# Kernel optimization log

Hardware: AMD Instinct MI355X
Metric: run time of the kernel (lower is better)

## Reference

```python
import jax, jax.numpy as jnp
import numpy as np

WINDOW_SIZE = 11
SIGMA = 1.5
LEVELS = 5
WEIGHTS = np.array([0.0448, 0.2856, 0.3001, 0.2363, 0.1333], dtype=np.float32)
C1 = 0.01 ** 2  # (0.01 * L)^2, L = 1
C2 = 0.03 ** 2


def _gauss_window(channel):
    x = np.arange(WINDOW_SIZE, dtype=np.float32) - WINDOW_SIZE // 2
    g = np.exp(-x ** 2 / (2.0 * SIGMA ** 2)).astype(np.float32)
    g = g / g.sum()
    w2 = np.outer(g, g)  # [ws, ws]
    w = np.broadcast_to(w2, (channel, 1, WINDOW_SIZE, WINDOW_SIZE)).copy()
    return jnp.asarray(w)


def _dwconv(x, w, channel):
    # depthwise conv, padding=0 (VALID), groups=channel
    return jax.lax.conv_general_dilated(
        x, w, window_strides=(1, 1), padding='VALID',
        dimension_numbers=('NCHW', 'OIHW', 'NCHW'),
        feature_group_count=channel)


def _ssim(img1, img2, window, channel):
    mu1 = _dwconv(img1, window, channel)
    mu2 = _dwconv(img2, window, channel)
    mu1_sq = mu1 * mu1
    mu2_sq = mu2 * mu2
    mu1_mu2 = mu1 * mu2
    sigma1_sq = _dwconv(img1 * img1, window, channel) - mu1_sq
    sigma2_sq = _dwconv(img2 * img2, window, channel) - mu2_sq
    sigma12 = _dwconv(img1 * img2, window, channel) - mu1_mu2
    v1 = 2.0 * sigma12 + C2
    v2 = sigma1_sq + sigma2_sq + C2
    cs = jnp.mean(v1 / v2)
    ssim_map = (2.0 * mu1_mu2 + C1) * v1 / ((mu1_sq + mu2_sq + C1) * v2)
    return jnp.mean(ssim_map), cs


def _avg_pool2(x):
    # avg_pool2d(kernel=2, stride=2), VALID
    s = jax.lax.reduce_window(x, 0.0, jax.lax.add, (1, 1, 2, 2), (1, 1, 2, 2), 'VALID')
    return s * 0.25


def setup_inputs() -> dict:
    key = jax.random.key(0)
    k1, k2 = jax.random.split(key)
    img1 = jax.random.uniform(k1, (16, 3, 512, 512), dtype=jnp.float32)
    img2 = jax.random.uniform(k2, (16, 3, 512, 512), dtype=jnp.float32)
    return {"img1": img1, "img2": img2}


def reference(img1, img2):
    channel = img1.shape[1]
    window = _gauss_window(channel)
    weights = jnp.asarray(WEIGHTS)
    mssim, mcs = [], []
    a, b = img1, img2
    for _ in range(LEVELS):  # fixed pyramid depth, shapes differ per level
        s, c = _ssim(a, b, window, channel)
        mssim.append(s)
        mcs.append(c)
        a = _avg_pool2(a)
        b = _avg_pool2(b)
    mssim = (jnp.stack(mssim) + 1.0) * 0.5  # normalize=True
    mcs = (jnp.stack(mcs) + 1.0) * 0.5
    return jnp.prod(mcs[:-1] ** weights[:-1]) * mssim[-1] ** weights[-1]
```

## Files before the change

### kernel.cpp

```cpp
#include <hip/hip_runtime.h>
#include <math.h>

#define WS 11
#define PAD 10
#define NC 48
#define C1V 1.0e-4f
#define C2V 9.0e-4f
#define PLROWS 42
#define RST 65

typedef float v2f __attribute__((ext_vector_type(2)));

struct Params { float g[WS]; };
struct ROff { int off[5]; int cnt[5]; float inv[5]; };

__device__ __forceinline__ void row_conv_unit(
    const float* __restrict__ rowa, const float* __restrict__ rowb,
    const int xq[4], int cg,
    v2f* __restrict__ rowSD, v2f* __restrict__ rowE2, const Params& P)
{
    v2f msd[4] = {{0,0},{0,0},{0,0},{0,0}};
    v2f me2[4] = {{0,0},{0,0},{0,0},{0,0}};
#pragma unroll
    for (int q = 0; q < 4; ++q) {
        const float4 va = *(const float4*)(rowa + xq[q]);
        const float4 vb = *(const float4*)(rowb + xq[q]);
        const float fa[4] = {va.x, va.y, va.z, va.w};
        const float fb[4] = {vb.x, vb.y, vb.z, vb.w};
#pragma unroll
        for (int e = 0; e < 4; ++e) {
            const int i = q * 4 + e;
            v2f sd; sd.x = fa[e] + fb[e]; sd.y = fa[e] - fb[e];
            const v2f sq = sd * sd;
#pragma unroll
            for (int j = 0; j < 4; ++j) {
                const int k = i - j;
                if (k >= 0 && k < WS) {
                    const float g = P.g[k];
                    msd[j] += g * sd;
                    me2[j] += g * sq;
                }
            }
        }
    }
#pragma unroll
    for (int j = 0; j < 4; ++j) {
        rowSD[cg*4 + j] = msd[j];
        rowE2[cg*4 + j] = me2[j];
    }
}

template<int CH, int POOL>
__global__ __launch_bounds__(512) void ssim_strip_kernel(
    const float* __restrict__ img1, const float* __restrict__ img2,
    float* __restrict__ pool1, float* __restrict__ pool2,
    int H, int OH, int tilesX, Params P,
    float2* __restrict__ partial, int partial_off)
{
    __shared__ v2f rpSD[PLROWS][RST];
    __shared__ v2f rpE2[PLROWS][RST];
    __shared__ float reds[8], redc[8];
    const int tid   = threadIdx.x;
    const int tileX = blockIdx.x % tilesX;
    const int ty    = blockIdx.x / tilesX;
    const int img   = blockIdx.y;
    const size_t ib = (size_t)img * H * H;
    const float* __restrict__ p1 = img1 + ib;
    const float* __restrict__ p2 = img2 + ib;
    const int ox0 = tileX * 64;
    const int oy0 = ty * (CH * 32);

    const int r_unit = tid >> 4;
    const int cg     = tid & 15;
    int xq[4];
#pragma unroll
    for (int q = 0; q < 4; ++q) xq[q] = min(ox0 + cg*4 + q*4, H - 4);

    const int cc  = tid & 63;
    const int r0c = (tid >> 6) * 4;

    if (tid < 160) {
        const int y = min(oy0 + r_unit, H - 1);
        row_conv_unit(p1 + (size_t)y*H, p2 + (size_t)y*H, xq, cg,
                      &rpSD[r_unit][0], &rpE2[r_unit][0], P);
    }

    float ssim_acc = 0.f, cs_acc = 0.f;

    for (int t = 0; t < CH; ++t) {
        {
            const int y = min(oy0 + t*32 + 10 + r_unit, H - 1);
            row_conv_unit(p1 + (size_t)y*H, p2 + (size_t)y*H, xq, cg,
                          &rpSD[10 + r_unit][0], &rpE2[10 + r_unit][0], P);
        }
        __syncthreads();

        v2f Asd[4] = {{0,0},{0,0},{0,0},{0,0}};
        v2f Ae2[4] = {{0,0},{0,0},{0,0},{0,0}};
        {
            v2f bsd[7], be2[7];
#pragma unroll
            for (int k = 0; k < 7; ++k) {
                bsd[k] = rpSD[r0c + k][cc];
                be2[k] = rpE2[r0c + k][cc];
            }
#pragma unroll
            for (int k = 0; k < 7; ++k) {
#pragma unroll
                for (int j = 0; j < 4; ++j) {
                    const int tt = k - j;
                    if (tt >= 0 && tt < WS) {
                        const float g = P.g[tt];
                        Asd[j] += g * bsd[k];
                        Ae2[j] += g * be2[k];
                    }
                }
            }
#pragma unroll
            for (int k = 7; k < 14; ++k) {
                bsd[k-7] = rpSD[r0c + k][cc];
                be2[k-7] = rpE2[r0c + k][cc];
            }
#pragma unroll
            for (int k = 7; k < 14; ++k) {
#pragma unroll
                for (int j = 0; j < 4; ++j) {
                    const int tt = k - j;
                    if (tt >= 0 && tt < WS) {
                        const float g = P.g[tt];
                        Asd[j] += g * bsd[k-7];
                        Ae2[j] += g * be2[k-7];
                    }
                }
            }
        }
        const int ox = ox0 + cc;
#pragma unroll
        for (int j = 0; j < 4; ++j) {
            const int oy = oy0 + t*32 + r0c + j;
            if (oy < OH && ox < OH) {
                const float ms = Asd[j].x, md = Asd[j].y;
                const float Es = Ae2[j].x, Ed = Ae2[j].y;
                const float ms2 = ms*ms, md2 = md*md;
                const float mu12 = 0.25f * (ms2 - md2);
                const float musq = 0.5f  * (ms2 + md2);
                const float v1 = 0.5f * (Es - Ed) - 2.f*mu12 + C2V;
                const float v2 = 0.5f * (Es + Ed) - musq + C2V;
                const float rv2 = __builtin_amdgcn_rcpf(v2);
                const float cs  = v1 * rv2;
                const float ssim = (2.f*mu12 + C1V) *
                                   __builtin_amdgcn_rcpf(musq + C1V) * cs;
                ssim_acc += ssim;
                cs_acc   += cs;
            }
        }

        if (POOL) {
            const int px = tid & 31, py = tid >> 5;
            const int yy = oy0 + t*32 + 2*py;
            const int xx = ox0 + 2*px;
            const float2 a0 = *(const float2*)(p1 + (size_t)yy*H + xx);
            const float2 a1 = *(const float2*)(p1 + (size_t)(yy+1)*H + xx);
            const float2 b0 = *(const float2*)(p2 + (size_t)yy*H + xx);
            const float2 b1 = *(const float2*)(p2 + (size_t)(yy+1)*H + xx);
            const int h = H >> 1;
            const size_t ob = (size_t)img*h*h +
                              (size_t)(((oy0 + t*32) >> 1) + py)*h + (ox0 >> 1) + px;
            pool1[ob] = 0.25f * (a0.x + a0.y + a1.x + a1.y);
            pool2[ob] = 0.25f * (b0.x + b0.y + b1.x + b1.y);
        }

        if (t + 1 < CH) {
            __syncthreads();
            for (int u = tid; u < 640; u += 512) {
                const int r = u >> 6, c = u & 63;
                rpSD[r][c] = rpSD[32 + r][c];
                rpE2[r][c] = rpE2[32 + r][c];
            }
            __syncthreads();
        }
    }

#pragma unroll
    for (int off = 32; off > 0; off >>= 1) {
        ssim_acc += __shfl_down(ssim_acc, off);
        cs_acc   += __shfl_down(cs_acc, off);
    }
    const int wave = tid >> 6, lane = tid & 63;
    if (lane == 0) { reds[wave] = ssim_acc; redc[wave] = cs_acc; }
    __syncthreads();
    if (tid == 0) {
        float s = 0.f, cc2 = 0.f;
#pragma unroll
        for (int w = 0; w < 8; ++w) { s += reds[w]; cc2 += redc[w]; }
        partial[(size_t)partial_off + (size_t)blockIdx.y * gridDim.x + blockIdx.x] =
            make_float2(s, cc2);
    }
}

__global__ __launch_bounds__(256) void reduce_final_kernel(
    const float2* __restrict__ partial, ROff ro, float* __restrict__ out)
{
    __shared__ float sS[5], sC[5];
    __shared__ float reds[4], redc[4];
    const int tid = threadIdx.x;
    for (int l = 0; l < 5; ++l) {
        float s = 0.f, c = 0.f;
        for (int i = tid; i < ro.cnt[l]; i += 256) {
            const float2 v = partial[ro.off[l] + i];
            s += v.x; c += v.y;
        }
#pragma unroll
        for (int off = 32; off > 0; off >>= 1) {
            s += __shfl_down(s, off);
            c += __shfl_down(c, off);
        }
        const int wave = tid >> 6, lane = tid & 63;
        if (lane == 0) { reds[wave] = s; redc[wave] = c; }
        __syncthreads();
        if (tid == 0) {
            sS[l] = (reds[0] + reds[1] + reds[2] + reds[3]) * ro.inv[l];
            sC[l] = (redc[0] + redc[1] + redc[2] + redc[3]) * ro.inv[l];
        }
        __syncthreads();
    }
    if (tid == 0) {
        const float w[5] = {0.0448f, 0.2856f, 0.3001f, 0.2363f, 0.1333f};
        float prod = 1.f;
#pragma unroll
        for (int i = 0; i < 4; ++i)
            prod *= powf((sC[i] + 1.f) * 0.5f, w[i]);
        prod *= powf((sS[4] + 1.f) * 0.5f, w[4]);
        out[0] = prod;
    }
}

extern "C" void kernel_launch(void* const* d_in, const int* in_sizes, int n_in,
                              void* d_out, int out_size, void* d_ws, size_t ws_size,
                              hipStream_t stream)
{
    const float* img1 = (const float*)d_in[0];
    const float* img2 = (const float*)d_in[1];
    float* out = (float*)d_out;
    float* ws  = (float*)d_ws;

    Params P;
    {
        double g[WS], sum = 0.0;
        for (int i = 0; i < WS; ++i) {
            double x = (double)i - (WS / 2);
            g[i] = exp(-x * x / (2.0 * 1.5 * 1.5));
            sum += g[i];
        }
        for (int i = 0; i < WS; ++i) P.g[i] = (float)(g[i] / sum);
    }

    float* p1[5]; float* p2[5];
    p1[0] = (float*)img1; p2[0] = (float*)img2;
    size_t o = 0;
    for (int l = 1; l < 5; ++l) {
        const int H = 512 >> l;
        p1[l] = ws + o; o += (size_t)NC * H * H;
        p2[l] = ws + o; o += (size_t)NC * H * H;
    }
    float2* partial = (float2*)(ws + o);
    (void)ws_size; (void)in_sizes; (void)n_in; (void)out_size;

    const int CHv[5] = {2, 2, 2, 2, 1};
    ROff ro;
    {
        int off = 0;
        for (int l = 0; l < 5; ++l) {
            const int H = 512 >> l, OH = H - PAD;
            const int tilesX = (OH + 63) / 64;
            const int tilesY = (OH + CHv[l]*32 - 1) / (CHv[l]*32);
            ro.off[l] = off;
            ro.cnt[l] = tilesX * tilesY * NC;
            ro.inv[l] = 1.f / ((float)NC * OH * OH);
            off += ro.cnt[l];
        }
    }

    for (int l = 0; l < 5; ++l) {
        const int H = 512 >> l, OH = H - PAD;
        const int tilesX = (OH + 63) / 64;
        const int tilesY = (OH + CHv[l]*32 - 1) / (CHv[l]*32);
        const dim3 grid(tilesX * tilesY, NC);
        if (l < 4)
            ssim_strip_kernel<2,1><<<grid, 512, 0, stream>>>(
                p1[l], p2[l], p1[l+1], p2[l+1], H, OH, tilesX, P, partial, ro.off[l]);
        else
            ssim_strip_kernel<1,0><<<grid, 512, 0, stream>>>(
                p1[4], p2[4], nullptr, nullptr, H, OH, tilesX, P, partial, ro.off[4]);
    }

    reduce_final_kernel<<<1, 256, 0, stream>>>(partial, ro, out);
}
```

Baseline: 116.5 us.

## Replace rolling strip kernel with independent 32x32 tiles and packed float4 LDS

Switches from 64-wide strips that process two 32-row chunks with a carried halo to independent 32x32 output tiles with 256-thread blocks. The row-convolution intermediates are packed into a single float4 shared array instead of two v2f arrays. This removes the halo copy and extra barriers and increases block count for parallelism, at the cost of more redundant halo row convolutions and global reads per output.

After: 109.2 us. 6.3% less time.

```diff
diff --git a/kernel.cpp b/kernel.cpp
--- a/kernel.cpp
+++ b/kernel.cpp
@@ -6,8 +6,8 @@
 #define NC 48
 #define C1V 1.0e-4f
 #define C2V 9.0e-4f
-#define PLROWS 42
-#define RST 65
+#define IH 42
+#define TW 32
 
 typedef float v2f __attribute__((ext_vector_type(2)));
 
@@ -16,8 +16,7 @@
 
 __device__ __forceinline__ void row_conv_unit(
     const float* __restrict__ rowa, const float* __restrict__ rowb,
-    const int xq[4], int cg,
-    v2f* __restrict__ rowSD, v2f* __restrict__ rowE2, const Params& P)
+    const int xq[4], int cg, float4* __restrict__ rprow, const Params& P)
 {
     v2f msd[4] = {{0,0},{0,0},{0,0},{0,0}};
     v2f me2[4] = {{0,0},{0,0},{0,0},{0,0}};
@@ -44,22 +43,19 @@
         }
     }
 #pragma unroll
-    for (int j = 0; j < 4; ++j) {
-        rowSD[cg*4 + j] = msd[j];
-        rowE2[cg*4 + j] = me2[j];
-    }
-}
-
-template<int CH, int POOL>
-__global__ __launch_bounds__(512) void ssim_strip_kernel(
+    for (int j = 0; j < 4; ++j)
+        rprow[cg*4 + j] = make_float4(msd[j].x, msd[j].y, me2[j].x, me2[j].y);
+}
+
+template<int POOL>
+__global__ __launch_bounds__(256) void ssim_tile_kernel(
     const float* __restrict__ img1, const float* __restrict__ img2,
     float* __restrict__ pool1, float* __restrict__ pool2,
     int H, int OH, int tilesX, Params P,
     float2* __restrict__ partial, int partial_off)
 {
-    __shared__ v2f rpSD[PLROWS][RST];
-    __shared__ v2f rpE2[PLROWS][RST];
-    __shared__ float reds[8], redc[8];
+    __shared__ float4 rp[IH][TW];
+    __shared__ float reds[4], redc[4];
     const int tid   = threadIdx.x;
     const int tileX = blockIdx.x % tilesX;
     const int ty    = blockIdx.x / tilesX;
@@ -67,118 +63,102 @@
     const size_t ib = (size_t)img * H * H;
     const float* __restrict__ p1 = img1 + ib;
     const float* __restrict__ p2 = img2 + ib;
-    const int ox0 = tileX * 64;
-    const int oy0 = ty * (CH * 32);
-
-    const int r_unit = tid >> 4;
-    const int cg     = tid & 15;
+    const int ox0 = tileX * TW;
+    const int oy0 = ty * TW;
+
+    const int r_unit = tid >> 3;
+    const int cg     = tid & 7;
     int xq[4];
 #pragma unroll
     for (int q = 0; q < 4; ++q) xq[q] = min(ox0 + cg*4 + q*4, H - 4);
 
-    const int cc  = tid & 63;
-    const int r0c = (tid >> 6) * 4;
-
-    if (tid < 160) {
+    const int cc  = tid & 31;
+    const int r0c = (tid >> 5) * 4;
+
+    {
         const int y = min(oy0 + r_unit, H - 1);
-        row_conv_unit(p1 + (size_t)y*H, p2 + (size_t)y*H, xq, cg,
-                      &rpSD[r_unit][0], &rpE2[r_unit][0], P);
-    }
-
-    float ssim_acc = 0.f, cs_acc = 0.f;
-
-    for (int t = 0; t < CH; ++t) {
-        {
-            const int y = min(oy0 + t*32 + 10 + r_unit, H - 1);
-            row_conv_unit(p1 + (size_t)y*H, p2 + (size_t)y*H, xq, cg,
-                          &rpSD[10 + r_unit][0], &rpE2[10 + r_unit][0], P);
-        }
-        __syncthreads();
-
-        v2f Asd[4] = {{0,0},{0,0},{0,0},{0,0}};
-        v2f Ae2[4] = {{0,0},{0,0},{0,0},{0,0}};
-        {
-            v2f bsd[7], be2[7];
-#pragma unroll
-            for (int k = 0; k < 7; ++k) {
-                bsd[k] = rpSD[r0c + k][cc];
-                be2[k] = rpE2[r0c + k][cc];
-            }
-#pragma unroll
-            for (int k = 0; k < 7; ++k) {
-#pragma unroll
-                for (int j = 0; j < 4; ++j) {
-                    const int tt = k - j;
-                    if (tt >= 0 && tt < WS) {
-                        const float g = P.g[tt];
-                        Asd[j] += g * bsd[k];
-                        Ae2[j] += g * be2[k];
-                    }
+        row_conv_unit(p1 + (size_t)y*H, p2 + (size_t)y*H, xq, cg, &rp[r_unit][0], P);
+    }
+    if (tid < 80) {
+        const int r2 = r_unit + 32;
+        const int y = min(oy0 + r2, H - 1);
+        row_conv_unit(p1 + (size_t)y*H, p2 + (size_t)y*H, xq, cg, &rp[r2][0], P);
+    }
+    __syncthreads();
+
+    v2f Asd[4] = {{0,0},{0,0},{0,0},{0,0}};
+    v2f Ae2[4] = {{0,0},{0,0},{0,0},{0,0}};
+    {
+        float4 b[7];
+#pragma unroll
+        for (int k = 0; k < 7; ++k) b[k] = rp[r0c + k][cc];
+#pragma unroll
+        for (int k = 0; k < 7; ++k) {
+            const v2f vsd = {b[k].x, b[k].y};
+            const v2f ve2 = {b[k].z, b[k].w};
+#pragma unroll
+            for (int j = 0; j < 4; ++j) {
+                const int tt = k - j;
+                if (tt >= 0 && tt < WS) {
+                    const float g = P.g[tt];
+                    Asd[j] += g * vsd;
+                    Ae2[j] += g * ve2;
                 }
             }
-#pragma unroll
-            for (int k = 7; k < 14; ++k) {
-                bsd[k-7] = rpSD[r0c + k][cc];
-                be2[k-7] = rpE2[r0c + k][cc];
-            }
-#pragma unroll
-            for (int k = 7; k < 14; ++k) {
-#pragma unroll
-                for (int j = 0; j < 4; ++j) {
-                    const int tt = k - j;
-                    if (tt >= 0 && tt < WS) {
-                        const float g = P.g[tt];
-                        Asd[j] += g * bsd[k-7];
-                        Ae2[j] += g * be2[k-7];
-                    }
+        }
+#pragma unroll
+        for (int k = 7; k < 14; ++k) b[k-7] = rp[r0c + k][cc];
+#pragma unroll
+        for (int k = 7; k < 14; ++k) {
+            const v2f vsd = {b[k-7].x, b[k-7].y};
+            const v2f ve2 = {b[k-7].z, b[k-7].w};
+#pragma unroll
+            for (int j = 0; j < 4; ++j) {
+                const int tt = k - j;
+                if (tt >= 0 && tt < WS) {
+                    const float g = P.g[tt];
+                    Asd[j] += g * vsd;
+                    Ae2[j] += g * ve2;
                 }
             }
         }
-        const int ox = ox0 + cc;
-#pragma unroll
-        for (int j = 0; j < 4; ++j) {
-            const int oy = oy0 + t*32 + r0c + j;
-            if (oy < OH && ox < OH) {
-                const float ms = Asd[j].x, md = Asd[j].y;
-                const float Es = Ae2[j].x, Ed = Ae2[j].y;
-                const float ms2 = ms*ms, md2 = md*md;
-                const float mu12 = 0.25f * (ms2 - md2);
-                const float musq = 0.5f  * (ms2 + md2);
-                const float v1 = 0.5f * (Es - Ed) - 2.f*mu12 + C2V;
-                const float v2 = 0.5f * (Es + Ed) - musq + C2V;
-                const float rv2 = __builtin_amdgcn_rcpf(v2);
-                const float cs  = v1 * rv2;
-                const float ssim = (2.f*mu12 + C1V) *
-                                   __builtin_amdgcn_rcpf(musq + C1V) * cs;
-                ssim_acc += ssim;
-                cs_acc   += cs;
-            }
-        }
-
-        if (POOL) {
-            const int px = tid & 31, py = tid >> 5;
-            const int yy = oy0 + t*32 + 2*py;
-            const int xx = ox0 + 2*px;
-            const float2 a0 = *(const float2*)(p1 + (size_t)yy*H + xx);
-            const float2 a1 = *(const float2*)(p1 + (size_t)(yy+1)*H + xx);
-            const float2 b0 = *(const float2*)(p2 + (size_t)yy*H + xx);
-            const float2 b1 = *(const float2*)(p2 + (size_t)(yy+1)*H + xx);
-            const int h = H >> 1;
-            const size_t ob = (size_t)img*h*h +
-                              (size_t)(((oy0 + t*32) >> 1) + py)*h + (ox0 >> 1) + px;
-            pool1[ob] = 0.25f * (a0.x + a0.y + a1.x + a1.y);
-            pool2[ob] = 0.25f * (b0.x + b0.y + b1.x + b1.y);
-        }
-
-        if (t + 1 < CH) {
-            __syncthreads();
-            for (int u = tid; u < 640; u += 512) {
-                const int r = u >> 6, c = u & 63;
-                rpSD[r][c] = rpSD[32 + r][c];
-                rpE2[r][c] = rpE2[32 + r][c];
-            }
-            __syncthreads();
-        }
+    }
+
+    float ssim_acc = 0.f, cs_acc = 0.f;
+    const int ox = ox0 + cc;
+#pragma unroll
+    for (int j = 0; j < 4; ++j) {
+        const int oy = oy0 + r0c + j;
+        if (oy < OH && ox < OH) {
+            const float ms = Asd[j].x, md = Asd[j].y;
+            const float Es = Ae2[j].x, Ed = Ae2[j].y;
+            const float ms2 = ms*ms, md2 = md*md;
+            const float mu12 = 0.25f * (ms2 - md2);
+            const float musq = 0.5f  * (ms2 + md2);
+            const float v1 = 0.5f * (Es - Ed) - 2.f*mu12 + C2V;
+            const float v2 = 0.5f * (Es + Ed) - musq + C2V;
+            const float rv2 = __builtin_amdgcn_rcpf(v2);
+            const float cs  = v1 * rv2;
+            const float ssim = (2.f*mu12 + C1V) *
+                               __builtin_amdgcn_rcpf(musq + C1V) * cs;
+            ssim_acc += ssim;
+            cs_acc   += cs;
+        }
+    }
+
+    if (POOL) {
+        const int px = tid & 15, py = tid >> 4;
+        const int yy = oy0 + 2*py;
+        const int xx = ox0 + 2*px;
+        const float2 a0 = *(const float2*)(p1 + (size_t)yy*H + xx);
+        const float2 a1 = *(const float2*)(p1 + (size_t)(yy+1)*H + xx);
+        const float2 b0 = *(const float2*)(p2 + (size_t)yy*H + xx);
+        const float2 b1 = *(const float2*)(p2 + (size_t)(yy+1)*H + xx);
+        const int h = H >> 1;
+        const size_t ob = (size_t)img*h*h +
+                          (size_t)((oy0 >> 1) + py)*h + (ox0 >> 1) + px;
+        pool1[ob] = 0.25f * (a0.x + a0.y + a1.x + a1.y);
+        pool2[ob] = 0.25f * (b0.x + b0.y + b1.x + b1.y);
     }
 
 #pragma unroll
@@ -190,9 +170,8 @@
     if (lane == 0) { reds[wave] = ssim_acc; redc[wave] = cs_acc; }
     __syncthreads();
     if (tid == 0) {
-        float s = 0.f, cc2 = 0.f;
-#pragma unroll
-        for (int w = 0; w < 8; ++w) { s += reds[w]; cc2 += redc[w]; }
+        const float s   = reds[0] + reds[1] + reds[2] + reds[3];
+        const float cc2 = redc[0] + redc[1] + redc[2] + redc[3];
         partial[(size_t)partial_off + (size_t)blockIdx.y * gridDim.x + blockIdx.x] =
             make_float2(s, cc2);
     }
@@ -266,16 +245,14 @@
     float2* partial = (float2*)(ws + o);
     (void)ws_size; (void)in_sizes; (void)n_in; (void)out_size;
 
-    const int CHv[5] = {2, 2, 2, 2, 1};
     ROff ro;
     {
         int off = 0;
         for (int l = 0; l < 5; ++l) {
             const int H = 512 >> l, OH = H - PAD;
-            const int tilesX = (OH + 63) / 64;
-            const int tilesY = (OH + CHv[l]*32 - 1) / (CHv[l]*32);
+            const int tiles = (OH + TW - 1) / TW;
             ro.off[l] = off;
-            ro.cnt[l] = tilesX * tilesY * NC;
+            ro.cnt[l] = tiles * tiles * NC;
             ro.inv[l] = 1.f / ((float)NC * OH * OH);
             off += ro.cnt[l];
         }
@@ -283,15 +260,14 @@
 
     for (int l = 0; l < 5; ++l) {
         const int H = 512 >> l, OH = H - PAD;
-        const int tilesX = (OH + 63) / 64;
-        const int tilesY = (OH + CHv[l]*32 - 1) / (CHv[l]*32);
-        const dim3 grid(tilesX * tilesY, NC);
+        const int tiles = (OH + TW - 1) / TW;
+        const dim3 grid(tiles * tiles, NC);
         if (l < 4)
-            ssim_strip_kernel<2,1><<<grid, 512, 0, stream>>>(
-                p1[l], p2[l], p1[l+1], p2[l+1], H, OH, tilesX, P, partial, ro.off[l]);
+            ssim_tile_kernel<1><<<grid, 256, 0, stream>>>(
+                p1[l], p2[l], p1[l+1], p2[l+1], H, OH, tiles, P, partial, ro.off[l]);
         else
-            ssim_strip_kernel<1,0><<<grid, 512, 0, stream>>>(
-                p1[4], p2[4], nullptr, nullptr, H, OH, tilesX, P, partial, ro.off[4]);
+            ssim_tile_kernel<0><<<grid, 256, 0, stream>>>(
+                p1[4], p2[4], nullptr, nullptr, H, OH, tiles, P, partial, ro.off[4]);
     }
 
     reduce_final_kernel<<<1, 256, 0, stream>>>(partial, ro, out);
```
